# Kernel optimization log

Measured on AMD Instinct MI355X. Metric: run time of the kernel, lower is better.

Reference implementation:

```python
import jax, jax.numpy as jnp
import numpy as np

B, N, M, D = 16, 128, 64, 512
H = 4
K = D // H  # head_dim = 128
L = 3      # num_labels


def setup_inputs() -> dict:
    key = jax.random.key(0)
    ks = jax.random.split(key, 16)
    s = 0.02
    return {
        "word": jax.random.normal(ks[0], (B, N, D), jnp.float32),
        "rel": jax.random.normal(ks[1], (B, M, D), jnp.float32),
        "mask": jnp.ones((B, M), jnp.float32),
        "Wn_w": jax.random.normal(ks[2], (D, D), jnp.float32) * s,
        "Wn_b": jnp.zeros((D,), jnp.float32),
        "Wr_w": jax.random.normal(ks[3], (D, D), jnp.float32) * s,
        "Wr_b": jnp.zeros((D,), jnp.float32),
        "lin_w": jax.random.normal(ks[4], (H, D, K), jnp.float32) * s,
        "lin_b": jnp.zeros((H, K), jnp.float32),
        "score_w": jax.random.normal(ks[5], (H, K), jnp.float32) * s,
        "score_b": jnp.zeros((H,), jnp.float32),
        "final_w": jax.random.normal(ks[6], (D, D), jnp.float32) * s,
        "final_b": jnp.zeros((D,), jnp.float32),
        "fc_w": jax.random.normal(ks[7], (D, L), jnp.float32) * s,
        "fc_b": jnp.zeros((L,), jnp.float32),
    }


def reference(word, rel, mask, Wn_w, Wn_b, Wr_w, Wr_b, lin_w, lin_b,
              score_w, score_b, final_w, final_b, fc_w, fc_b):
    # projections (dropout = identity in eval mode)
    w = word @ Wn_w + Wn_b                     # [B,N,D]
    r = rel @ Wr_w + Wr_b                      # [B,M,D]
    # outer-product hadamard + relu            # [B,N,M,D]
    had = jax.nn.relu(w[:, :, None, :] * r[:, None, :, :])
    # per-head linear projection, vectorized over heads
    t = jnp.einsum('bnmd,hdk->bnmhk', had, lin_w) + lin_b  # [B,N,M,H,K]
    # per-head scalar score + softmax over M (the dim=-1 of [B,N,M])
    s = jnp.einsum('bnmhk,hk->bnmh', t, score_w) + score_b  # [B,N,M,H]
    wts = jax.nn.softmax(s, axis=2) * mask[:, None, :, None]
    # masked weighted sum over M, then mean over N
    head = jnp.einsum('bnmh,bnmhk->bnhk', wts, t)           # [B,N,H,K]
    head = head.mean(axis=1).reshape(head.shape[0], H * K)  # [B,D] (concat heads)
    out = head @ final_w + final_b
    out = jax.nn.relu(out)
    logits = out @ fc_w + fc_b                               # [B,L]
    return logits
```

## Files before the change

kernel.cpp:

```cpp
#include <hip/hip_runtime.h>
#include <math.h>


#define OFF_W   0
#define OFF_R   (2048*512)
#define OFF_V   (OFF_R + 1024*512)
#define OFF_S   (OFF_V + 2048)
#define OFF_G   (OFF_S + 16*4*64*128)
#define OFF_SW  (OFF_G + 16*4*512)
#define OFF_HM  (OFF_SW + 128)
#define OFF_OS  (OFF_HM + 16*512)

__global__ __launch_bounds__(256) void proj_gemm(
    const float* __restrict__ word, const float* __restrict__ rel,
    const float* __restrict__ Wn_w, const float* __restrict__ Wn_b,
    const float* __restrict__ Wr_w, const float* __restrict__ Wr_b,
    float* __restrict__ ws)
{
    int blk = blockIdx.x;
    const float *A, *W, *bias;
    float* C;
    int rowTile, colTile;
    if (blk < 256) {
        A = word; W = Wn_w; bias = Wn_b; C = ws + OFF_W;
        rowTile = blk >> 3; colTile = blk & 7;
    } else {
        int b2 = blk - 256;
        A = rel; W = Wr_w; bias = Wr_b; C = ws + OFF_R;
        rowTile = b2 >> 3; colTile = b2 & 7;
    }
    const int row0 = rowTile * 64, col0 = colTile * 64;

    __shared__ float As[16][68];
    __shared__ float Bs[16][64];

    const int t  = threadIdx.x;
    const int tx = t & 15, ty = t >> 4;
    const int lr = t >> 2, lk = (t & 3) << 2;
    const int bk = t >> 4, bc = (t & 15) << 2;

    float acc[4][4] = {};

    for (int k0 = 0; k0 < 512; k0 += 16) {
        float4 a4 = *(const float4*)(A + (size_t)(row0 + lr) * 512 + k0 + lk);
        As[lk + 0][lr] = a4.x; As[lk + 1][lr] = a4.y;
        As[lk + 2][lr] = a4.z; As[lk + 3][lr] = a4.w;
        *(float4*)&Bs[bk][bc] = *(const float4*)(W + (size_t)(k0 + bk) * 512 + col0 + bc);
        __syncthreads();
        #pragma unroll
        for (int kk = 0; kk < 16; kk++) {
            float4 av = *(float4*)&As[kk][ty << 2];
            float4 bv = *(float4*)&Bs[kk][tx << 2];
            float aa[4] = {av.x, av.y, av.z, av.w};
            float bb[4] = {bv.x, bv.y, bv.z, bv.w};
            #pragma unroll
            for (int i = 0; i < 4; i++)
                #pragma unroll
                for (int j = 0; j < 4; j++)
                    acc[i][j] = fmaf(aa[i], bb[j], acc[i][j]);
        }
        __syncthreads();
    }
    float4 bv = *(const float4*)(bias + col0 + (tx << 2));
    float bb[4] = {bv.x, bv.y, bv.z, bv.w};
    #pragma unroll
    for (int i = 0; i < 4; i++) {
        float4 o;
        o.x = acc[i][0] + bb[0]; o.y = acc[i][1] + bb[1];
        o.z = acc[i][2] + bb[2]; o.w = acc[i][3] + bb[3];
        *(float4*)(C + (size_t)(row0 + (ty << 2) + i) * 512 + col0 + (tx << 2)) = o;
    }
}

__global__ __launch_bounds__(256) void prep_v(
    const float* __restrict__ lin_w, const float* __restrict__ score_w,
    float* __restrict__ ws)
{
    int gid = blockIdx.x * 256 + threadIdx.x;
    int h = gid >> 9, d = gid & 511;
    const float* lw = lin_w + (size_t)(h * 512 + d) * 128;
    const float* sw = score_w + h * 128;
    float acc = 0.f;
    #pragma unroll 4
    for (int k = 0; k < 128; k += 4) {
        float4 a = *(const float4*)(lw + k);
        float4 b = *(const float4*)(sw + k);
        acc = fmaf(a.x, b.x, acc); acc = fmaf(a.y, b.y, acc);
        acc = fmaf(a.z, b.z, acc); acc = fmaf(a.w, b.w, acc);
    }
    ws[OFF_V + h * 512 + d] = 0.5f * acc;
}

__global__ __launch_bounds__(256) void scores_kernel(float* __restrict__ ws)
{
    const int blk = blockIdx.x;
    const int mhtile = blk & 3;
    const int ntile  = (blk >> 2) & 3;
    const int b      = blk >> 4;
    const int n0 = ntile * 32;
    const int m0 = mhtile * 16;

    const float* wbase = ws + OFF_W + (size_t)(b * 128) * 512;
    const float* rbase = ws + OFF_R + (size_t)(b * 64) * 512;
    float* sbase = ws + OFF_S + (size_t)(b * 4) * 8192;

    __shared__ float v2s[2048];
    __shared__ float Asab[16][68];
    __shared__ float Bs[16][68];
    __shared__ float Ba[16][68];

    const int t = threadIdx.x;
    #pragma unroll
    for (int i = 0; i < 2; i++) {
        int idx4 = t + i * 256;
        *(float4*)&v2s[idx4 * 4] = *(const float4*)(ws + OFF_V + idx4 * 4);
    }
    __syncthreads();

    const int tx = t & 15, ty = t >> 4;
    const int an = t >> 3;
    const int ak = (t & 7) * 2;
    const int bk = t & 15;
    const int bq = t >> 4;

    float acc[2][4] = {};

    for (int k0 = 0; k0 < 512; k0 += 16) {
        float2 a2 = *(const float2*)(wbase + (size_t)(n0 + an) * 512 + k0 + ak);
        Asab[ak    ][an * 2]     = a2.x;
        Asab[ak    ][an * 2 + 1] = fabsf(a2.x);
        Asab[ak + 1][an * 2]     = a2.y;
        Asab[ak + 1][an * 2 + 1] = fabsf(a2.y);
        float rv = rbase[(size_t)(m0 + bq) * 512 + k0 + bk];
        float ra = fabsf(rv);
        #pragma unroll
        for (int h = 0; h < 4; h++) {
            float vv = v2s[h * 512 + k0 + bk];
            Bs[bk][bq * 4 + h] = rv * vv;
            Ba[bk][bq * 4 + h] = ra * vv;
        }
        __syncthreads();
        #pragma unroll
        for (int kk = 0; kk < 16; kk++) {
            float4 a  = *(float4*)&Asab[kk][ty * 4];
            float4 bs = *(float4*)&Bs[kk][tx * 4];
            float4 ba = *(float4*)&Ba[kk][tx * 4];
            float bsv[4] = {bs.x, bs.y, bs.z, bs.w};
            float bav[4] = {ba.x, ba.y, ba.z, ba.w};
            #pragma unroll
            for (int j = 0; j < 4; j++) {
                acc[0][j] = fmaf(a.x, bsv[j], acc[0][j]);
                acc[0][j] = fmaf(a.y, bav[j], acc[0][j]);
                acc[1][j] = fmaf(a.z, bsv[j], acc[1][j]);
                acc[1][j] = fmaf(a.w, bav[j], acc[1][j]);
            }
        }
        __syncthreads();
    }
    #pragma unroll
    for (int i = 0; i < 2; i++)
        #pragma unroll
        for (int j = 0; j < 4; j++)
            sbase[((size_t)j * 64 + m0 + tx) * 128 + n0 + ty * 2 + i] = acc[i][j];
}

__global__ __launch_bounds__(256) void softmax_kernel(
    const float* __restrict__ mask, float* __restrict__ ws)
{
    const int blk = blockIdx.x;
    const int nh = blk & 1, bh = blk >> 1, b = bh >> 2;
    float* sbase = ws + OFF_S + (size_t)bh * 8192;

    __shared__ float sl[64][68];
    __shared__ float maskl[64];

    const int t = threadIdx.x;
    if (t < 64) maskl[t] = mask[b * 64 + t];
    #pragma unroll
    for (int i = 0; i < 4; i++) {
        int idx4 = t + i * 256;
        int row = idx4 >> 4, col = (idx4 & 15) * 4;
        *(float4*)&sl[row][col] = *(const float4*)(sbase + (size_t)row * 128 + nh * 64 + col);
    }
    __syncthreads();

    if (t < 64) {
        const int n = t;
        float e[64];
        float mx = -1e30f;
        #pragma unroll
        for (int m = 0; m < 64; m++) { e[m] = sl[m][n]; mx = fmaxf(mx, e[m]); }
        float sum = 0.f;
        #pragma unroll
        for (int m = 0; m < 64; m++) { e[m] = expf(e[m] - mx); sum += e[m]; }
        float inv = 1.0f / sum;
        float colsum = 0.f;
        #pragma unroll
        for (int m = 0; m < 64; m++) {
            float wt = e[m] * inv * maskl[m];
            sl[m][n] = wt;
            colsum += wt;
        }
        #pragma unroll
        for (int off = 32; off > 0; off >>= 1)
            colsum += __shfl_xor(colsum, off);
        if (t == 0) ws[OFF_SW + blk] = colsum;
    }
    __syncthreads();
    #pragma unroll
    for (int i = 0; i < 4; i++) {
        int idx4 = t + i * 256;
        int row = idx4 >> 4, col = (idx4 & 15) * 4;
        *(float4*)(sbase + (size_t)row * 128 + nh * 64 + col) = *(float4*)&sl[row][col];
    }
}

__global__ __launch_bounds__(256) void gstep_kernel(float* __restrict__ ws)
{
    const int blk = blockIdx.x;
    const int dtile = blk & 7, bh = blk >> 3;
    const int b = bh >> 2;
    const int d0 = dtile * 64;
    const float* wts   = ws + OFF_S + (size_t)bh * 8192;
    const float* wbase = ws + OFF_W + (size_t)(b * 128) * 512;
    const float* rbase = ws + OFF_R + (size_t)(b * 64) * 512;

    __shared__ float As[16][68];
    __shared__ float Bs[16][68];
    __shared__ float Ba[16][68];
    __shared__ float red[16][68];

    const int t = threadIdx.x;
    const int tx = t & 15, ty = t >> 4;
    const int am = t >> 2, an4 = (t & 3) * 4;
    const int bn = t >> 4, bd4 = (t & 15) * 4;

    float accC[4][4] = {}, accA[4][4] = {};

    for (int n0 = 0; n0 < 128; n0 += 16) {
        float4 a4 = *(const float4*)(wts + (size_t)am * 128 + n0 + an4);
        As[an4 + 0][am] = a4.x; As[an4 + 1][am] = a4.y;
        As[an4 + 2][am] = a4.z; As[an4 + 3][am] = a4.w;
        float4 b4 = *(const float4*)(wbase + (size_t)(n0 + bn) * 512 + d0 + bd4);
        *(float4*)&Bs[bn][bd4] = b4;
        float4 bb; bb.x = fabsf(b4.x); bb.y = fabsf(b4.y);
        bb.z = fabsf(b4.z); bb.w = fabsf(b4.w);
        *(float4*)&Ba[bn][bd4] = bb;
        __syncthreads();
        #pragma unroll
        for (int kk = 0; kk < 16; kk++) {
            float4 av  = *(float4*)&As[kk][ty * 4];
            float4 bv  = *(float4*)&Bs[kk][tx * 4];
            float4 bav = *(float4*)&Ba[kk][tx * 4];
            float av_[4]  = {av.x, av.y, av.z, av.w};
            float bv_[4]  = {bv.x, bv.y, bv.z, bv.w};
            float bav_[4] = {bav.x, bav.y, bav.z, bav.w};
            #pragma unroll
            for (int i = 0; i < 4; i++)
                #pragma unroll
                for (int j = 0; j < 4; j++) {
                    accC[i][j] = fmaf(av_[i], bv_[j],  accC[i][j]);
                    accA[i][j] = fmaf(av_[i], bav_[j], accA[i][j]);
                }
        }
        __syncthreads();
    }
    float g0 = 0.f, g1 = 0.f, g2 = 0.f, g3 = 0.f;
    #pragma unroll
    for (int i = 0; i < 4; i++) {
        float4 rv = *(const float4*)(rbase + (size_t)(ty * 4 + i) * 512 + d0 + tx * 4);
        g0 = fmaf(rv.x, accC[i][0], g0); g0 = fmaf(fabsf(rv.x), accA[i][0], g0);
        g1 = fmaf(rv.y, accC[i][1], g1); g1 = fmaf(fabsf(rv.y), accA[i][1], g1);
        g2 = fmaf(rv.z, accC[i][2], g2); g2 = fmaf(fabsf(rv.z), accA[i][2], g2);
        g3 = fmaf(rv.w, accC[i][3], g3); g3 = fmaf(fabsf(rv.w), accA[i][3], g3);
    }
    float4 gg; gg.x = g0; gg.y = g1; gg.z = g2; gg.w = g3;
    *(float4*)&red[ty][tx * 4] = gg;
    __syncthreads();
    if (t < 64) {
        float s = 0.f;
        #pragma unroll
        for (int q = 0; q < 16; q++) s += red[q][t];
        ws[OFF_G + (size_t)bh * 512 + d0 + t] = 0.5f * s;
    }
}

__global__ __launch_bounds__(256) void headmean_kernel(
    const float* __restrict__ lin_w, const float* __restrict__ lin_b,
    float* __restrict__ ws)
{
    const int bh = blockIdx.x, b = bh >> 2, h = bh & 3;
    __shared__ float Gs[512];
    __shared__ float red[128];
    const int t = threadIdx.x;
    Gs[t]       = ws[OFF_G + (size_t)bh * 512 + t];
    Gs[t + 256] = ws[OFF_G + (size_t)bh * 512 + t + 256];
    __syncthreads();
    const float SWv = ws[OFF_SW + bh * 2] + ws[OFF_SW + bh * 2 + 1];
    const int k = t & 127, half = t >> 7;
    const float* lwp = lin_w + ((size_t)h * 512 + half * 256) * 128 + k;
    const float* gp = Gs + half * 256;
    float acc = 0.f;
    #pragma unroll 8
    for (int d = 0; d < 256; d++)
        acc = fmaf(gp[d], lwp[(size_t)d * 128], acc);
    if (half) red[k] = acc;
    __syncthreads();
    if (!half) {
        float tot = acc + red[k] + lin_b[h * 128 + k] * SWv;
        ws[OFF_HM + (size_t)b * 512 + h * 128 + k] = tot * (1.0f / 128.0f);
    }
}

__global__ __launch_bounds__(256) void final_kernel(
    const float* __restrict__ final_w, const float* __restrict__ final_b,
    float* __restrict__ ws)
{
    const int blk = blockIdx.x, b = blk >> 2, jt = blk & 3;
    __shared__ float hs[512];
    __shared__ float red[128];
    const int t = threadIdx.x;
    hs[t]       = ws[OFF_HM + (size_t)b * 512 + t];
    hs[t + 256] = ws[OFF_HM + (size_t)b * 512 + t + 256];
    __syncthreads();
    const int k = t & 127, half = t >> 7;
    const int j = jt * 128 + k;
    const float* fwp = final_w + (size_t)(half * 256) * 512 + j;
    const float* hp = hs + half * 256;
    float acc = 0.f;
    #pragma unroll 8
    for (int d = 0; d < 256; d++)
        acc = fmaf(hp[d], fwp[(size_t)d * 512], acc);
    if (half) red[k] = acc;
    __syncthreads();
    if (!half) {
        float o = fmaxf(acc + red[k] + final_b[j], 0.f);
        ws[OFF_OS + (size_t)b * 512 + j] = o;
    }
}

__global__ __launch_bounds__(192) void logits_kernel(
    const float* __restrict__ fc_w, const float* __restrict__ fc_b,
    const float* __restrict__ ws, float* __restrict__ out)
{
    const int b = blockIdx.x, t = threadIdx.x;
    const int l = t >> 6, ln = t & 63;
    const float* os = ws + OFF_OS + (size_t)b * 512;
    float acc = 0.f;
    for (int i = ln; i < 512; i += 64)
        acc = fmaf(os[i], fc_w[i * 3 + l], acc);
    #pragma unroll
    for (int off = 32; off > 0; off >>= 1)
        acc += __shfl_xor(acc, off);
    if (ln == 0) out[b * 3 + l] = acc + fc_b[l];
}

extern "C" void kernel_launch(void* const* d_in, const int* in_sizes, int n_in,
                              void* d_out, int out_size, void* d_ws, size_t ws_size,
                              hipStream_t stream)
{
    const float* word    = (const float*)d_in[0];
    const float* rel     = (const float*)d_in[1];
    const float* mask    = (const float*)d_in[2];
    const float* Wn_w    = (const float*)d_in[3];
    const float* Wn_b    = (const float*)d_in[4];
    const float* Wr_w    = (const float*)d_in[5];
    const float* Wr_b    = (const float*)d_in[6];
    const float* lin_w   = (const float*)d_in[7];
    const float* lin_b   = (const float*)d_in[8];
    const float* score_w = (const float*)d_in[9];
    const float* final_w = (const float*)d_in[11];
    const float* final_b = (const float*)d_in[12];
    const float* fc_w    = (const float*)d_in[13];
    const float* fc_b    = (const float*)d_in[14];
    float* ws  = (float*)d_ws;
    float* out = (float*)d_out;

    proj_gemm<<<384, 256, 0, stream>>>(word, rel, Wn_w, Wn_b, Wr_w, Wr_b, ws);
    prep_v<<<8, 256, 0, stream>>>(lin_w, score_w, ws);
    scores_kernel<<<256, 256, 0, stream>>>(ws);
    softmax_kernel<<<128, 256, 0, stream>>>(mask, ws);
    gstep_kernel<<<512, 256, 0, stream>>>(ws);
    headmean_kernel<<<64, 256, 0, stream>>>(lin_w, lin_b, ws);
    final_kernel<<<64, 256, 0, stream>>>(final_w, final_b, ws);
    logits_kernel<<<16, 192, 0, stream>>>(fc_w, fc_b, ws, out);
}
```

Baseline: 207.8 us.

## Fuse pipeline into fewer kernels: scores+softmax, final+logits, prep into proj

Folds the prep_v work into extra blocks of the projection GEMM, and fuses the score GEMM with the softmax per (b,h,n-quarter) so the weights go out already transposed. It also widens headmean and final to 256 blocks with 8-way split-K reductions, and fuses final with logits using atomicAdd into a pre-zeroed output. The aim is to cut launch count and intermediate global round trips and to raise parallelism in the small tail kernels. The cost is an added memset and atomics, and the score GEMM is now recomputed per head with a smaller tile.

```diff
diff --git a/kernel.cpp b/kernel.cpp
--- a/kernel.cpp
+++ b/kernel.cpp
@@ -6,18 +6,34 @@
 #define OFF_R   (2048*512)
 #define OFF_V   (OFF_R + 1024*512)
 #define OFF_S   (OFF_V + 2048)
-#define OFF_G   (OFF_S + 16*4*64*128)
-#define OFF_SW  (OFF_G + 16*4*512)
-#define OFF_HM  (OFF_SW + 128)
-#define OFF_OS  (OFF_HM + 16*512)
+#define OFF_G   (OFF_S + 64*8192)
+#define OFF_SW  (OFF_G + 64*512)
+#define OFF_HM  (OFF_SW + 256)
 
 __global__ __launch_bounds__(256) void proj_gemm(
     const float* __restrict__ word, const float* __restrict__ rel,
     const float* __restrict__ Wn_w, const float* __restrict__ Wn_b,
     const float* __restrict__ Wr_w, const float* __restrict__ Wr_b,
+    const float* __restrict__ lin_w, const float* __restrict__ score_w,
     float* __restrict__ ws)
 {
     int blk = blockIdx.x;
+    if (blk >= 384) {
+        int gid = (blk - 384) * 256 + threadIdx.x;
+        int h = gid >> 9, d = gid & 511;
+        const float* lw = lin_w + (size_t)(h * 512 + d) * 128;
+        const float* sw = score_w + h * 128;
+        float acc = 0.f;
+        #pragma unroll 4
+        for (int k = 0; k < 128; k += 4) {
+            float4 a = *(const float4*)(lw + k);
+            float4 b = *(const float4*)(sw + k);
+            acc = fmaf(a.x, b.x, acc); acc = fmaf(a.y, b.y, acc);
+            acc = fmaf(a.z, b.z, acc); acc = fmaf(a.w, b.w, acc);
+        }
+        ws[OFF_V + h * 512 + d] = 0.5f * acc;
+        return;
+    }
     const float *A, *W, *bias;
     float* C;
     int rowTile, colTile;
@@ -72,147 +88,111 @@
     }
 }
 
-__global__ __launch_bounds__(256) void prep_v(
-    const float* __restrict__ lin_w, const float* __restrict__ score_w,
-    float* __restrict__ ws)
-{
-    int gid = blockIdx.x * 256 + threadIdx.x;
-    int h = gid >> 9, d = gid & 511;
-    const float* lw = lin_w + (size_t)(h * 512 + d) * 128;
-    const float* sw = score_w + h * 128;
-    float acc = 0.f;
-    #pragma unroll 4
-    for (int k = 0; k < 128; k += 4) {
-        float4 a = *(const float4*)(lw + k);
-        float4 b = *(const float4*)(sw + k);
-        acc = fmaf(a.x, b.x, acc); acc = fmaf(a.y, b.y, acc);
-        acc = fmaf(a.z, b.z, acc); acc = fmaf(a.w, b.w, acc);
-    }
-    ws[OFF_V + h * 512 + d] = 0.5f * acc;
-}
-
-__global__ __launch_bounds__(256) void scores_kernel(float* __restrict__ ws)
+__global__ __launch_bounds__(256) void scores_sm(
+    const float* __restrict__ mask, float* __restrict__ ws)
 {
     const int blk = blockIdx.x;
-    const int mhtile = blk & 3;
-    const int ntile  = (blk >> 2) & 3;
-    const int b      = blk >> 4;
-    const int n0 = ntile * 32;
-    const int m0 = mhtile * 16;
+    const int nq = blk & 3, bh = blk >> 2, h = bh & 3, b = bh >> 2;
+    const int n0 = nq * 32;
 
     const float* wbase = ws + OFF_W + (size_t)(b * 128) * 512;
     const float* rbase = ws + OFF_R + (size_t)(b * 64) * 512;
-    float* sbase = ws + OFF_S + (size_t)(b * 4) * 8192;
-
-    __shared__ float v2s[2048];
-    __shared__ float Asab[16][68];
-    __shared__ float Bs[16][68];
-    __shared__ float Ba[16][68];
+    float* wtsT = ws + OFF_S + (size_t)bh * 8192;
+
+    __shared__ float v2s[512];
+    __shared__ float maskl[64];
+    __shared__ float As[16][68], Aa[16][68];
+    __shared__ float Bs[16][36], Ba[16][36];
+    __shared__ float sl[64][37];
+    __shared__ float invl[33];
 
     const int t = threadIdx.x;
-    #pragma unroll
-    for (int i = 0; i < 2; i++) {
-        int idx4 = t + i * 256;
-        *(float4*)&v2s[idx4 * 4] = *(const float4*)(ws + OFF_V + idx4 * 4);
-    }
-    __syncthreads();
-
-    const int tx = t & 15, ty = t >> 4;
-    const int an = t >> 3;
-    const int ak = (t & 7) * 2;
-    const int bk = t & 15;
-    const int bq = t >> 4;
-
-    float acc[2][4] = {};
+    if (t < 128) *(float4*)&v2s[t * 4] = *(const float4*)(ws + OFF_V + h * 512 + t * 4);
+    if (t < 64) maskl[t] = mask[b * 64 + t];
+    __syncthreads();
+
+    const int ty = t >> 4, tx = t & 15;
+    const int am = t >> 2, akq = (t & 3) * 4;
+    const int bn = t >> 2, bkq = (t & 3) * 4;
+
+    float acc[4][2] = {};
 
     for (int k0 = 0; k0 < 512; k0 += 16) {
-        float2 a2 = *(const float2*)(wbase + (size_t)(n0 + an) * 512 + k0 + ak);
-        Asab[ak    ][an * 2]     = a2.x;
-        Asab[ak    ][an * 2 + 1] = fabsf(a2.x);
-        Asab[ak + 1][an * 2]     = a2.y;
-        Asab[ak + 1][an * 2 + 1] = fabsf(a2.y);
-        float rv = rbase[(size_t)(m0 + bq) * 512 + k0 + bk];
-        float ra = fabsf(rv);
-        #pragma unroll
-        for (int h = 0; h < 4; h++) {
-            float vv = v2s[h * 512 + k0 + bk];
-            Bs[bk][bq * 4 + h] = rv * vv;
-            Ba[bk][bq * 4 + h] = ra * vv;
+        {
+            float4 r4 = *(const float4*)(rbase + (size_t)am * 512 + k0 + akq);
+            float4 vv = *(const float4*)&v2s[k0 + akq];
+            As[akq + 0][am] = r4.x * vv.x; Aa[akq + 0][am] = fabsf(r4.x) * vv.x;
+            As[akq + 1][am] = r4.y * vv.y; Aa[akq + 1][am] = fabsf(r4.y) * vv.y;
+            As[akq + 2][am] = r4.z * vv.z; Aa[akq + 2][am] = fabsf(r4.z) * vv.z;
+            As[akq + 3][am] = r4.w * vv.w; Aa[akq + 3][am] = fabsf(r4.w) * vv.w;
+        }
+        if (t < 128) {
+            float4 w4 = *(const float4*)(wbase + (size_t)(n0 + bn) * 512 + k0 + bkq);
+            Bs[bkq + 0][bn] = w4.x; Ba[bkq + 0][bn] = fabsf(w4.x);
+            Bs[bkq + 1][bn] = w4.y; Ba[bkq + 1][bn] = fabsf(w4.y);
+            Bs[bkq + 2][bn] = w4.z; Ba[bkq + 2][bn] = fabsf(w4.z);
+            Bs[bkq + 3][bn] = w4.w; Ba[bkq + 3][bn] = fabsf(w4.w);
         }
         __syncthreads();
         #pragma unroll
         for (int kk = 0; kk < 16; kk++) {
-            float4 a  = *(float4*)&Asab[kk][ty * 4];
-            float4 bs = *(float4*)&Bs[kk][tx * 4];
-            float4 ba = *(float4*)&Ba[kk][tx * 4];
-            float bsv[4] = {bs.x, bs.y, bs.z, bs.w};
-            float bav[4] = {ba.x, ba.y, ba.z, ba.w};
+            float4 a  = *(float4*)&As[kk][ty * 4];
+            float4 aa = *(float4*)&Aa[kk][ty * 4];
+            float2 bv  = *(float2*)&Bs[kk][tx * 2];
+            float2 bav = *(float2*)&Ba[kk][tx * 2];
+            float a_[4]  = {a.x, a.y, a.z, a.w};
+            float aa_[4] = {aa.x, aa.y, aa.z, aa.w};
             #pragma unroll
-            for (int j = 0; j < 4; j++) {
-                acc[0][j] = fmaf(a.x, bsv[j], acc[0][j]);
-                acc[0][j] = fmaf(a.y, bav[j], acc[0][j]);
-                acc[1][j] = fmaf(a.z, bsv[j], acc[1][j]);
-                acc[1][j] = fmaf(a.w, bav[j], acc[1][j]);
+            for (int i = 0; i < 4; i++) {
+                acc[i][0] = fmaf(a_[i], bv.x,  acc[i][0]);
+                acc[i][0] = fmaf(aa_[i], bav.x, acc[i][0]);
+                acc[i][1] = fmaf(a_[i], bv.y,  acc[i][1]);
+                acc[i][1] = fmaf(aa_[i], bav.y, acc[i][1]);
             }
         }
         __syncthreads();
     }
-    #pragma unroll
-    for (int i = 0; i < 2; i++)
-        #pragma unroll
-        for (int j = 0; j < 4; j++)
-            sbase[((size_t)j * 64 + m0 + tx) * 128 + n0 + ty * 2 + i] = acc[i][j];
-}
-
-__global__ __launch_bounds__(256) void softmax_kernel(
-    const float* __restrict__ mask, float* __restrict__ ws)
-{
-    const int blk = blockIdx.x;
-    const int nh = blk & 1, bh = blk >> 1, b = bh >> 2;
-    float* sbase = ws + OFF_S + (size_t)bh * 8192;
-
-    __shared__ float sl[64][68];
-    __shared__ float maskl[64];
-
-    const int t = threadIdx.x;
-    if (t < 64) maskl[t] = mask[b * 64 + t];
     #pragma unroll
     for (int i = 0; i < 4; i++) {
-        int idx4 = t + i * 256;
-        int row = idx4 >> 4, col = (idx4 & 15) * 4;
-        *(float4*)&sl[row][col] = *(const float4*)(sbase + (size_t)row * 128 + nh * 64 + col);
-    }
-    __syncthreads();
-
-    if (t < 64) {
+        sl[ty * 4 + i][tx * 2 + 0] = acc[i][0];
+        sl[ty * 4 + i][tx * 2 + 1] = acc[i][1];
+    }
+    __syncthreads();
+
+    if (t < 32) {
         const int n = t;
-        float e[64];
-        float mx = -1e30f;
-        #pragma unroll
-        for (int m = 0; m < 64; m++) { e[m] = sl[m][n]; mx = fmaxf(mx, e[m]); }
-        float sum = 0.f;
-        #pragma unroll
-        for (int m = 0; m < 64; m++) { e[m] = expf(e[m] - mx); sum += e[m]; }
-        float inv = 1.0f / sum;
-        float colsum = 0.f;
+        float mx = sl[0][n];
+        #pragma unroll
+        for (int m = 1; m < 64; m++) mx = fmaxf(mx, sl[m][n]);
+        float esum = 0.f, emsum = 0.f;
         #pragma unroll
         for (int m = 0; m < 64; m++) {
-            float wt = e[m] * inv * maskl[m];
-            sl[m][n] = wt;
-            colsum += wt;
-        }
-        #pragma unroll
-        for (int off = 32; off > 0; off >>= 1)
-            colsum += __shfl_xor(colsum, off);
-        if (t == 0) ws[OFF_SW + blk] = colsum;
-    }
-    __syncthreads();
+            float e = expf(sl[m][n] - mx);
+            sl[m][n] = e;
+            esum += e;
+            emsum = fmaf(e, maskl[m], emsum);
+        }
+        float inv = 1.0f / esum;
+        invl[n] = inv;
+        float swq = emsum * inv;
+        #pragma unroll
+        for (int off = 16; off > 0; off >>= 1)
+            swq += __shfl_xor(swq, off);
+        if (t == 0) ws[OFF_SW + bh * 4 + nq] = swq;
+    }
+    __syncthreads();
+
+    const int wn = t >> 3;
+    const int wm = (t & 7) * 8;
+    const float inv = invl[wn];
+    float o[8];
     #pragma unroll
-    for (int i = 0; i < 4; i++) {
-        int idx4 = t + i * 256;
-        int row = idx4 >> 4, col = (idx4 & 15) * 4;
-        *(float4*)(sbase + (size_t)row * 128 + nh * 64 + col) = *(float4*)&sl[row][col];
-    }
+    for (int e2 = 0; e2 < 8; e2++)
+        o[e2] = sl[wm + e2][wn] * inv * maskl[wm + e2];
+    float4 o0; o0.x = o[0]; o0.y = o[1]; o0.z = o[2]; o0.w = o[3];
+    float4 o1; o1.x = o[4]; o1.y = o[5]; o1.z = o[6]; o1.w = o[7];
+    *(float4*)(wtsT + (size_t)(n0 + wn) * 64 + wm)     = o0;
+    *(float4*)(wtsT + (size_t)(n0 + wn) * 64 + wm + 4) = o1;
 }
 
 __global__ __launch_bounds__(256) void gstep_kernel(float* __restrict__ ws)
@@ -221,7 +201,7 @@
     const int dtile = blk & 7, bh = blk >> 3;
     const int b = bh >> 2;
     const int d0 = dtile * 64;
-    const float* wts   = ws + OFF_S + (size_t)bh * 8192;
+    const float* wtsT  = ws + OFF_S + (size_t)bh * 8192;
     const float* wbase = ws + OFF_W + (size_t)(b * 128) * 512;
     const float* rbase = ws + OFF_R + (size_t)(b * 64) * 512;
 
@@ -232,15 +212,14 @@
 
     const int t = threadIdx.x;
     const int tx = t & 15, ty = t >> 4;
-    const int am = t >> 2, an4 = (t & 3) * 4;
+    const int an_r = t >> 4, am4 = (t & 15) * 4;
     const int bn = t >> 4, bd4 = (t & 15) * 4;
 
     float accC[4][4] = {}, accA[4][4] = {};
 
     for (int n0 = 0; n0 < 128; n0 += 16) {
-        float4 a4 = *(const float4*)(wts + (size_t)am * 128 + n0 + an4);
-        As[an4 + 0][am] = a4.x; As[an4 + 1][am] = a4.y;
-        As[an4 + 2][am] = a4.z; As[an4 + 3][am] = a4.w;
+        *(float4*)&As[an_r][am4] =
+            *(const float4*)(wtsT + (size_t)(n0 + an_r) * 64 + am4);
         float4 b4 = *(const float4*)(wbase + (size_t)(n0 + bn) * 512 + d0 + bd4);
         *(float4*)&Bs[bn][bd4] = b4;
         float4 bb; bb.x = fabsf(b4.x); bb.y = fabsf(b4.y);
@@ -289,70 +268,81 @@
     const float* __restrict__ lin_w, const float* __restrict__ lin_b,
     float* __restrict__ ws)
 {
-    const int bh = blockIdx.x, b = bh >> 2, h = bh & 3;
+    const int blk = blockIdx.x;
+    const int kt = blk & 3, bh = blk >> 2, b = bh >> 2, h = bh & 3;
+    const int t = threadIdx.x;
+    const int dg = t >> 5, kk = t & 31;
+    const int k = kt * 32 + kk;
+
     __shared__ float Gs[512];
-    __shared__ float red[128];
-    const int t = threadIdx.x;
+    __shared__ float red[8][33];
+
     Gs[t]       = ws[OFF_G + (size_t)bh * 512 + t];
     Gs[t + 256] = ws[OFF_G + (size_t)bh * 512 + t + 256];
     __syncthreads();
-    const float SWv = ws[OFF_SW + bh * 2] + ws[OFF_SW + bh * 2 + 1];
-    const int k = t & 127, half = t >> 7;
-    const float* lwp = lin_w + ((size_t)h * 512 + half * 256) * 128 + k;
-    const float* gp = Gs + half * 256;
+
+    const float* lwp = lin_w + ((size_t)h * 512 + dg * 64) * 128 + k;
+    const float* gp = Gs + dg * 64;
     float acc = 0.f;
     #pragma unroll 8
-    for (int d = 0; d < 256; d++)
+    for (int d = 0; d < 64; d++)
         acc = fmaf(gp[d], lwp[(size_t)d * 128], acc);
-    if (half) red[k] = acc;
-    __syncthreads();
-    if (!half) {
-        float tot = acc + red[k] + lin_b[h * 128 + k] * SWv;
-        ws[OFF_HM + (size_t)b * 512 + h * 128 + k] = tot * (1.0f / 128.0f);
-    }
-}
-
-__global__ __launch_bounds__(256) void final_kernel(
+    red[dg][kk] = acc;
+    __syncthreads();
+    if (t < 32) {
+        float s = 0.f;
+        #pragma unroll
+        for (int q = 0; q < 8; q++) s += red[q][t];
+        const float SWv = ws[OFF_SW + bh * 4 + 0] + ws[OFF_SW + bh * 4 + 1]
+                        + ws[OFF_SW + bh * 4 + 2] + ws[OFF_SW + bh * 4 + 3];
+        s = fmaf(lin_b[h * 128 + kt * 32 + t], SWv, s);
+        ws[OFF_HM + (size_t)b * 512 + h * 128 + kt * 32 + t] = s * (1.0f / 128.0f);
+    }
+}
+
+__global__ __launch_bounds__(256) void final_logits(
     const float* __restrict__ final_w, const float* __restrict__ final_b,
-    float* __restrict__ ws)
-{
-    const int blk = blockIdx.x, b = blk >> 2, jt = blk & 3;
+    const float* __restrict__ fc_w, const float* __restrict__ fc_b,
+    const float* __restrict__ ws, float* __restrict__ out)
+{
+    const int blk = blockIdx.x;
+    const int jt = blk & 15, b = blk >> 4;
+    const int t = threadIdx.x;
+    const int dg = t >> 5, jj = t & 31;
+    const int j = jt * 32 + jj;
+
     __shared__ float hs[512];
-    __shared__ float red[128];
-    const int t = threadIdx.x;
+    __shared__ float red[8][33];
+    __shared__ float osl[32];
+
     hs[t]       = ws[OFF_HM + (size_t)b * 512 + t];
     hs[t + 256] = ws[OFF_HM + (size_t)b * 512 + t + 256];
     __syncthreads();
-    const int k = t & 127, half = t >> 7;
-    const int j = jt * 128 + k;
-    const float* fwp = final_w + (size_t)(half * 256) * 512 + j;
-    const float* hp = hs + half * 256;
+
+    const float* fwp = final_w + (size_t)(dg * 64) * 512 + j;
+    const float* hp = hs + dg * 64;
     float acc = 0.f;
     #pragma unroll 8
-    for (int d = 0; d < 256; d++)
+    for (int d = 0; d < 64; d++)
         acc = fmaf(hp[d], fwp[(size_t)d * 512], acc);
-    if (half) red[k] = acc;
-    __syncthreads();
-    if (!half) {
-        float o = fmaxf(acc + red[k] + final_b[j], 0.f);
-        ws[OFF_OS + (size_t)b * 512 + j] = o;
-    }
-}
-
-__global__ __launch_bounds__(192) void logits_kernel(
-    const float* __restrict__ fc_w, const float* __restrict__ fc_b,
-    const float* __restrict__ ws, float* __restrict__ out)
-{
-    const int b = blockIdx.x, t = threadIdx.x;
-    const int l = t >> 6, ln = t & 63;
-    const float* os = ws + OFF_OS + (size_t)b * 512;
-    float acc = 0.f;
-    for (int i = ln; i < 512; i += 64)
-        acc = fmaf(os[i], fc_w[i * 3 + l], acc);
-    #pragma unroll
-    for (int off = 32; off > 0; off >>= 1)
-        acc += __shfl_xor(acc, off);
-    if (ln == 0) out[b * 3 + l] = acc + fc_b[l];
+    red[dg][jj] = acc;
+    __syncthreads();
+    if (t < 32) {
+        float s = 0.f;
+        #pragma unroll
+        for (int q = 0; q < 8; q++) s += red[q][t];
+        osl[t] = fmaxf(s + final_b[jt * 32 + t], 0.f);
+    }
+    __syncthreads();
+    if (t < 96) {
+        const int l = t >> 5, j2 = t & 31;
+        float val = osl[j2] * fc_w[(jt * 32 + j2) * 3 + l];
+        #pragma unroll
+        for (int off = 16; off > 0; off >>= 1)
+            val += __shfl_xor(val, off);
+        if (j2 == 0) atomicAdd(out + b * 3 + l, val);
+    }
+    if (jt == 0 && t < 3) atomicAdd(out + b * 3 + t, fc_b[t]);
 }
 
 extern "C" void kernel_launch(void* const* d_in, const int* in_sizes, int n_in,
@@ -376,12 +366,12 @@
     float* ws  = (float*)d_ws;
     float* out = (float*)d_out;
 
-    proj_gemm<<<384, 256, 0, stream>>>(word, rel, Wn_w, Wn_b, Wr_w, Wr_b, ws);
-    prep_v<<<8, 256, 0, stream>>>(lin_w, score_w, ws);
-    scores_kernel<<<256, 256, 0, stream>>>(ws);
-    softmax_kernel<<<128, 256, 0, stream>>>(mask, ws);
+    hipMemsetAsync(out, 0, 16 * 3 * sizeof(float), stream);
+
+    proj_gemm<<<392, 256, 0, stream>>>(word, rel, Wn_w, Wn_b, Wr_w, Wr_b,
+                                       lin_w, score_w, ws);
+    scores_sm<<<256, 256, 0, stream>>>(mask, ws);
     gstep_kernel<<<512, 256, 0, stream>>>(ws);
-    headmean_kernel<<<64, 256, 0, stream>>>(lin_w, lin_b, ws);
-    final_kernel<<<64, 256, 0, stream>>>(final_w, final_b, ws);
-    logits_kernel<<<16, 192, 0, stream>>>(fc_w, fc_b, ws, out);
-}
+    headmean_kernel<<<256, 256, 0, stream>>>(lin_w, lin_b, ws);
+    final_logits<<<256, 256, 0, stream>>>(final_w, final_b, fc_w, fc_b, ws, out);
+}
```

Result: faster. 191.2 us (-8.0%).
